# Kernel tuning notes

Hardware: AMD Instinct MI355X
Metric: run time of the kernel (lower is better)

Reference implementation:

```python
import jax, jax.numpy as jnp
import numpy as np

B, Q, N, C = 2, 1024, 4096, 768
H, D, REL = 12, 64, 32
SCALE = 1.0 / np.sqrt(D)


def _lin_coords(n_out, n_in):
    # align_corners=True mapping: x_in = x_out * (n_in-1)/(n_out-1)
    pos = jnp.arange(n_out, dtype=jnp.float32) * ((n_in - 1) / (n_out - 1))
    lo = jnp.clip(jnp.floor(pos).astype(jnp.int32), 0, n_in - 1)
    hi = jnp.clip(lo + 1, 0, n_in - 1)
    w = pos - lo.astype(jnp.float32)
    return lo, hi, w


def _interp_bias(bias, q_len, n_len):
    # bias: [H, 32, 32] -> [H, q_len, n_len] bilinear, align_corners=True
    lq, hq, wq = _lin_coords(q_len, REL)
    ln, hn, wn = _lin_coords(n_len, REL)
    b1 = bias[:, lq, :] * (1.0 - wq)[None, :, None] + bias[:, hq, :] * wq[None, :, None]  # [H,q,32]
    b2 = b1[:, :, ln] * (1.0 - wn)[None, None, :] + b1[:, :, hn] * wn[None, None, :]      # [H,q,n]
    return b2


def setup_inputs() -> dict:
    key = jax.random.key(0)
    ks = jax.random.split(key, 11)
    s = 1.0 / np.sqrt(C)
    return {
        "query": jax.random.normal(ks[0], (B, Q, C), jnp.float32),
        "key_value": jax.random.normal(ks[1], (B, N, C), jnp.float32),
        "Wq": jax.random.normal(ks[2], (C, C), jnp.float32) * s,
        "bq": jax.random.normal(ks[3], (C,), jnp.float32) * 0.01,
        "Wk": jax.random.normal(ks[4], (C, C), jnp.float32) * s,
        "bk": jax.random.normal(ks[5], (C,), jnp.float32) * 0.01,
        "Wv": jax.random.normal(ks[6], (C, C), jnp.float32) * s,
        "bv": jax.random.normal(ks[7], (C,), jnp.float32) * 0.01,
        "Wo": jax.random.normal(ks[8], (C, C), jnp.float32) * s,
        "bo": jax.random.normal(ks[9], (C,), jnp.float32) * 0.01,
        "rel_pos_bias": jax.random.normal(ks[10], (H, REL, REL), jnp.float32) * 0.02,
    }


def reference(query, key_value, Wq, bq, Wk, bk, Wv, bv, Wo, bo, rel_pos_bias):
    b, n, c = key_value.shape
    q_len = query.shape[1]
    # projections (dropout in eval mode -> identity)
    q = (query @ Wq + bq).reshape(b, q_len, H, D).transpose(0, 2, 1, 3)      # [B,H,Q,D]
    k = (key_value @ Wk + bk).reshape(b, n, H, D).transpose(0, 2, 1, 3)      # [B,H,N,D]
    v = (key_value @ Wv + bv).reshape(b, n, H, D).transpose(0, 2, 1, 3)      # [B,H,N,D]
    attn = jnp.einsum('bhqd,bhnd->bhqn', q, k) * SCALE
    attn = attn + _interp_bias(rel_pos_bias, q_len, n)[None]                 # [B,H,Q,N]
    p = jax.nn.softmax(attn, axis=-1)
    out = jnp.einsum('bhqn,bhnd->bhqd', p, v)
    out = out.transpose(0, 2, 1, 3).reshape(b, q_len, c)
    return out @ Wo + bo
```

## Files before the change

kernel.cpp:

```cpp
#include <hip/hip_runtime.h>
#include <stdint.h>

typedef unsigned short ushort_t;
typedef __bf16 bf16x8 __attribute__((ext_vector_type(8)));
typedef float f32x4 __attribute__((ext_vector_type(4)));
typedef unsigned short us4 __attribute__((ext_vector_type(4)));

#define LOG2E 1.4426950408889634f
#define NEG8L (-11.541560327111707f)
#define QSCALE 0.18033688011110974f

__device__ __forceinline__ ushort_t f2b(float f) {
    unsigned u = __float_as_uint(f);
    unsigned r = (u + 0x7fffu + ((u >> 16) & 1u)) >> 16;
    return (ushort_t)r;
}
__device__ __forceinline__ void gld16(const void* g, void* l) {
    __builtin_amdgcn_global_load_lds(
        (__attribute__((address_space(1))) void*)g,
        (__attribute__((address_space(3))) void*)l,
        16, 0, 0);
}

__global__ __launch_bounds__(256) void prep(
        const float* __restrict__ query, const float* __restrict__ keyv,
        const float* __restrict__ Wq, const float* __restrict__ Wk,
        const float* __restrict__ Wv, const float* __restrict__ Wo,
        const float* __restrict__ rel,
        ushort_t* __restrict__ qc, ushort_t* __restrict__ kvc,
        ushort_t* __restrict__ wtq, ushort_t* __restrict__ wtk,
        ushort_t* __restrict__ wtv, ushort_t* __restrict__ wto,
        ushort_t* __restrict__ b1b, ushort_t* __restrict__ wtab) {
    __shared__ ushort_t tsh[32][33];
    const int bid = blockIdx.x, tid = threadIdx.x;
    if (bid < 7680) {
        const float* src = (bid < 1536) ? query : keyv;
        ushort_t* dst = (bid < 1536) ? qc : kvc;
        int i = ((bid < 1536) ? bid : bid - 1536) * 256 + tid;
        float4 x = ((const float4*)src)[i];
        us4 v; v.x = f2b(x.x); v.y = f2b(x.y); v.z = f2b(x.z); v.w = f2b(x.w);
        ((us4*)dst)[i] = v;
    } else if (bid < 9984) {
        int t = bid - 7680, w = t / 576, tt = t - w * 576;
        const float* in = (w == 0) ? Wq : (w == 1) ? Wk : (w == 2) ? Wv : Wo;
        ushort_t* out = (w == 0) ? wtq : (w == 1) ? wtk : (w == 2) ? wtv : wto;
        int x = tid & 31, y = tid >> 5;
        int bx = (tt % 24) * 32, by = (tt / 24) * 32;
#pragma unroll
        for (int j = 0; j < 32; j += 8)
            tsh[y + j][x] = f2b(in[(size_t)(by + y + j) * 768 + bx + x]);
        __syncthreads();
#pragma unroll
        for (int j = 0; j < 32; j += 8)
            out[(size_t)(bx + y + j) * 768 + by + x] = tsh[x][y + j];
    } else if (bid < 11520) {
        int idx = (bid - 9984) * 256 + tid;
        int j = idx & 31, q = (idx >> 5) & 1023, h = idx >> 15;
        float pos = q * (31.0f / 1023.0f);
        float fl = floorf(pos);
        int lo = (int)fl; if (lo > 31) lo = 31;
        float w = pos - fl;
        int hi = lo + 1; if (hi > 31) hi = 31;
        float vlo = rel[(h * 32 + lo) * 32 + j];
        float vhi = rel[(h * 32 + hi) * 32 + j];
        b1b[idx] = f2b((vlo + (vhi - vlo) * w) * LOG2E);
    } else {
        int n = (bid - 11520) * 256 + tid;
        float pos = n * (31.0f / 4095.0f);
        float fl = floorf(pos);
        int ln = (int)fl; if (ln > 31) ln = 31;
        float wn = pos - fl;
        int hn = ln + 1; if (hn > 31) hn = 31;
        float vals[32];
#pragma unroll
        for (int j = 0; j < 32; ++j) vals[j] = 0.f;
        vals[ln] += 1.0f - wn;
        vals[hn] += wn;
#pragma unroll
        for (int j = 0; j < 32; ++j) wtab[n * 32 + j] = f2b(vals[j]);
    }
}

__device__ __forceinline__ void gemm_store(float bvf, f32x4 a, void* out,
                                           int mode, int lsh, float scale,
                                           int mbase, int n) {
    if (mode == 0) {
#pragma unroll
        for (int r = 0; r < 4; ++r)
            ((float*)out)[(size_t)(mbase + r) * 768 + n] = (a[r] + bvf) * scale;
    } else if (mode == 1) {
        int h = n >> 6, d = n & 63;
#pragma unroll
        for (int r = 0; r < 4; ++r) {
            int m = mbase + r;
            int b = m >> lsh, l = m & ((1 << lsh) - 1);
            ((ushort_t*)out)[((size_t)(((b * 12 + h) << lsh) + l) << 6) + d] = f2b((a[r] + bvf) * scale);
        }
    } else {
        int h = n >> 6, d = n & 63;
        int b = mbase >> lsh, l = mbase & ((1 << lsh) - 1);
        us4 v;
        v.x = f2b((a[0] + bvf) * scale);
        v.y = f2b((a[1] + bvf) * scale);
        v.z = f2b((a[2] + bvf) * scale);
        v.w = f2b((a[3] + bvf) * scale);
        *(us4*)((ushort_t*)out + ((size_t)((b * 12 + h) * 64 + d) << lsh) + l) = v;
    }
}

__device__ __forceinline__ void gemm_body128(const ushort_t* __restrict__ A,
                                             const ushort_t* __restrict__ Bt,
                                             const float* __restrict__ bias,
                                             void* __restrict__ out,
                                             int mode, int lsh, float scale,
                                             int m0, int n0,
                                             ushort_t* As, ushort_t* Bs, int tid) {
    const int wave = tid >> 6, lane = tid & 63;
    const int quad = lane >> 4, l15 = lane & 15;
    const int wm = wave >> 1, wn = wave & 1;
    const f32x4 z4 = {0.f, 0.f, 0.f, 0.f};
    f32x4 acc[4][4];
#pragma unroll
    for (int i = 0; i < 4; ++i)
#pragma unroll
        for (int j = 0; j < 4; ++j) acc[i][j] = z4;

    const int arow = lane >> 3;
    const int ablk = lane & 7;
    const int kswz = (ablk ^ arow) * 8;

    for (int kk = 0; kk < 768; kk += 64) {
        __syncthreads();
#pragma unroll
        for (int i = 0; i < 4; ++i) {
            int c = wave * 4 + i;
            gld16(A + (size_t)(m0 + c * 8 + arow) * 768 + kk + kswz, (void*)(As + c * 512));
            gld16(Bt + (size_t)(n0 + c * 8 + arow) * 768 + kk + kswz, (void*)(Bs + c * 512));
        }
        __syncthreads();
#pragma unroll
        for (int ks = 0; ks < 2; ++ks) {
            bf16x8 af[4], bf[4];
#pragma unroll
            for (int mb = 0; mb < 4; ++mb) {
                int r = wm * 64 + mb * 16 + l15;
                af[mb] = *(const bf16x8*)(As + r * 64 + (((ks * 4 + quad) ^ (r & 7)) * 8));
            }
#pragma unroll
            for (int nb = 0; nb < 4; ++nb) {
                int r = wn * 64 + nb * 16 + l15;
                bf[nb] = *(const bf16x8*)(Bs + r * 64 + (((ks * 4 + quad) ^ (r & 7)) * 8));
            }
#pragma unroll
            for (int mb = 0; mb < 4; ++mb)
#pragma unroll
                for (int nb = 0; nb < 4; ++nb)
                    acc[mb][nb] = __builtin_amdgcn_mfma_f32_16x16x32_bf16(af[mb], bf[nb], acc[mb][nb], 0, 0, 0);
        }
    }

#pragma unroll
    for (int mb = 0; mb < 4; ++mb) {
        int mbase = m0 + wm * 64 + mb * 16 + quad * 4;
#pragma unroll
        for (int nb = 0; nb < 4; ++nb) {
            int n = n0 + wn * 64 + nb * 16 + l15;
            gemm_store(bias[n], acc[mb][nb], out, mode, lsh, scale, mbase, n);
        }
    }
}

__device__ __forceinline__ void gemm_body64(const ushort_t* __restrict__ A,
                                            const ushort_t* __restrict__ Bt,
                                            const float* __restrict__ bias,
                                            void* __restrict__ out,
                                            int mode, int lsh, float scale,
                                            int m0, int n0,
                                            ushort_t* As, ushort_t* Bs, int tid) {
    const int wave = tid >> 6, lane = tid & 63;
    const int quad = lane >> 4, l15 = lane & 15;
    const f32x4 z4 = {0.f, 0.f, 0.f, 0.f};
    f32x4 acc[4];
#pragma unroll
    for (int j = 0; j < 4; ++j) acc[j] = z4;

    const int arow = lane >> 3;
    const int ablk = lane & 7;
    const int kswz = (ablk ^ arow) * 8;

    for (int kk = 0; kk < 768; kk += 64) {
        __syncthreads();
#pragma unroll
        for (int i = 0; i < 2; ++i) {
            int c = wave * 2 + i;
            gld16(A + (size_t)(m0 + c * 8 + arow) * 768 + kk + kswz, (void*)(As + c * 512));
            gld16(Bt + (size_t)(n0 + c * 8 + arow) * 768 + kk + kswz, (void*)(Bs + c * 512));
        }
        __syncthreads();
#pragma unroll
        for (int ks = 0; ks < 2; ++ks) {
            bf16x8 af, bf[4];
            {
                int r = wave * 16 + l15;
                af = *(const bf16x8*)(As + r * 64 + (((ks * 4 + quad) ^ (r & 7)) * 8));
            }
#pragma unroll
            for (int nb = 0; nb < 4; ++nb) {
                int r = nb * 16 + l15;
                bf[nb] = *(const bf16x8*)(Bs + r * 64 + (((ks * 4 + quad) ^ (r & 7)) * 8));
            }
#pragma unroll
            for (int nb = 0; nb < 4; ++nb)
                acc[nb] = __builtin_amdgcn_mfma_f32_16x16x32_bf16(af, bf[nb], acc[nb], 0, 0, 0);
        }
    }

    int mbase = m0 + wave * 16 + quad * 4;
#pragma unroll
    for (int nb = 0; nb < 4; ++nb) {
        int n = n0 + nb * 16 + l15;
        gemm_store(bias[n], acc[nb], out, mode, lsh, scale, mbase, n);
    }
}

__global__ __launch_bounds__(256) void proj3(const ushort_t* __restrict__ qc,
                                             const ushort_t* __restrict__ kvc,
                                             const ushort_t* __restrict__ wtq,
                                             const ushort_t* __restrict__ wtk,
                                             const ushort_t* __restrict__ wtv,
                                             const float* __restrict__ bq,
                                             const float* __restrict__ bk,
                                             const float* __restrict__ bv,
                                             ushort_t* __restrict__ qp,
                                             ushort_t* __restrict__ kp,
                                             ushort_t* __restrict__ vtp) {
    __shared__ __align__(16) ushort_t As[128 * 64];
    __shared__ __align__(16) ushort_t Bs[128 * 64];
    const int bid = blockIdx.x, tid = threadIdx.x;
    if (bid < 96) {
        int mt = bid & 15, nt = bid >> 4;
        gemm_body128(qc, wtq, bq, qp, 1, 10, QSCALE, mt * 128, nt * 128, As, Bs, tid);
    } else if (bid < 480) {
        int t = bid - 96, mt = t & 63, nt = t >> 6;
        gemm_body128(kvc, wtk, bk, kp, 1, 12, 1.0f, mt * 128, nt * 128, As, Bs, tid);
    } else {
        int t = bid - 480, mt = t & 63, nt = t >> 6;
        gemm_body128(kvc, wtv, bv, vtp, 2, 12, 1.0f, mt * 128, nt * 128, As, Bs, tid);
    }
}

__global__ __launch_bounds__(256) void gemm_out(const ushort_t* __restrict__ ab,
                                                const ushort_t* __restrict__ wto,
                                                const float* __restrict__ bo,
                                                float* __restrict__ out) {
    __shared__ __align__(16) ushort_t As[64 * 64];
    __shared__ __align__(16) ushort_t Bs[64 * 64];
    const int bid = blockIdx.x, tid = threadIdx.x;
    int mt = bid & 31, nt = bid >> 5;
    gemm_body64(ab, wto, bo, out, 0, 0, 1.0f, mt * 64, nt * 64, As, Bs, tid);
}

__global__ __launch_bounds__(256) void attn64s(const ushort_t* __restrict__ qp,
                                               const ushort_t* __restrict__ kp,
                                               const ushort_t* __restrict__ vt,
                                               const ushort_t* __restrict__ b1b,
                                               const ushort_t* __restrict__ wtab,
                                               float* __restrict__ po,
                                               float* __restrict__ pl) {
    __shared__ __align__(16) ushort_t k_s[64 * 64];
    __shared__ __align__(16) ushort_t v_s[64 * 64];
    __shared__ __align__(16) float pf[4][576];

    const int tid = threadIdx.x;
    const int wave = tid >> 6, lane = tid & 63;
    const int quad = lane >> 4, l15 = lane & 15;
    const int bid = blockIdx.x;
    const int xcd = bid & 7;
    const int slot = bid >> 3;
    const int g = xcd + 8 * (slot >> 6);
    const int member = slot & 63;
    const int b = g / 12, h = g - b * 12;
    const int qt = member & 15, sp = member >> 4;
    const int q0 = qt * 64;
    const int bh = g;

    const ushort_t* qg = qp + ((size_t)bh * 1024 + q0) * 64;
    const ushort_t* kg = kp + (size_t)bh * 4096 * 64;
    const ushort_t* vg = vt + (size_t)bh * 64 * 4096;

    const int rowq = wave * 16 + l15;
    bf16x8 aq[2];
#pragma unroll
    for (int ks = 0; ks < 2; ++ks)
        aq[ks] = *(const bf16x8*)(qg + (size_t)rowq * 64 + (ks * 4 + quad) * 8);
    bf16x8 ab1 = *(const bf16x8*)(b1b + ((size_t)(h * 1024 + q0 + rowq)) * 32 + quad * 8);

    const f32x4 mC = {NEG8L, NEG8L, NEG8L, NEG8L};
    const f32x4 z4 = {0.f, 0.f, 0.f, 0.f};
    f32x4 o[4];
    float lsum[4];
#pragma unroll
    for (int d = 0; d < 4; ++d) o[d] = z4;
#pragma unroll
    for (int r = 0; r < 4; ++r) lsum[r] = 0.f;

    const int arow = lane >> 3;
    const int ablk = lane & 7;

    for (int nt = 0; nt < 16; ++nt) {
        const int n0 = sp * 1024 + nt * 64;
        __syncthreads();
#pragma unroll
        for (int i = 0; i < 2; ++i) {
            int c = wave * 2 + i;
            int row = c * 8 + arow;
            int k16 = ablk ^ (row & 7);
            gld16(kg + (size_t)(n0 + row) * 64 + k16 * 8, (void*)(k_s + c * 512));
            gld16(vg + (size_t)row * 4096 + n0 + k16 * 8, (void*)(v_s + c * 512));
        }
        __syncthreads();

        bf16x8 wf[4];
#pragma unroll
        for (int nb = 0; nb < 4; ++nb)
            wf[nb] = *(const bf16x8*)(wtab + (size_t)(n0 + nb * 16 + l15) * 32 + quad * 8);

        f32x4 s[4];
#pragma unroll
        for (int nb = 0; nb < 4; ++nb) {
            s[nb] = __builtin_amdgcn_mfma_f32_16x16x32_bf16(ab1, wf[nb], mC, 0, 0, 0);
#pragma unroll
            for (int ks = 0; ks < 2; ++ks) {
                int rn = nb * 16 + l15;
                bf16x8 bk = *(const bf16x8*)(k_s + rn * 64 + (((ks * 4 + quad) ^ (rn & 7)) * 8));
                s[nb] = __builtin_amdgcn_mfma_f32_16x16x32_bf16(aq[ks], bk, s[nb], 0, 0, 0);
            }
        }
#pragma unroll
        for (int nb = 0; nb < 4; ++nb)
#pragma unroll
            for (int r = 0; r < 4; ++r) {
                float p = exp2f(s[nb][r]);
                s[nb][r] = p;
                lsum[r] += p;
            }
#pragma unroll
        for (int p = 0; p < 2; ++p) {
#pragma unroll
            for (int i = 0; i < 2; ++i) {
                int nb = 2 * p + i;
                float* dst = &pf[wave][(i * 16 + l15) * 18 + quad * 4];
                *(float2*)dst = make_float2(s[nb][0], s[nb][1]);
                *(float2*)(dst + 2) = make_float2(s[nb][2], s[nb][3]);
            }
            bf16x8 ap;
#pragma unroll
            for (int j = 0; j < 8; ++j)
                ap[j] = (__bf16)pf[wave][(quad * 8 + j) * 18 + l15];
#pragma unroll
            for (int d = 0; d < 4; ++d) {
                int rd = d * 16 + l15;
                bf16x8 bv = *(const bf16x8*)(v_s + rd * 64 + (((p * 4 + quad) ^ (rd & 7)) * 8));
                o[d] = __builtin_amdgcn_mfma_f32_16x16x32_bf16(ap, bv, o[d], 0, 0, 0);
            }
        }
    }

#pragma unroll
    for (int r = 0; r < 4; ++r)
#pragma unroll
        for (int off = 1; off < 16; off <<= 1)
            lsum[r] += __shfl_xor(lsum[r], off, 64);

    const size_t pbase = ((size_t)(sp * 24 + bh)) * 1024;
#pragma unroll
    for (int r = 0; r < 4; ++r) {
        int qrow = q0 + wave * 16 + quad * 4 + r;
        if (l15 == 0) pl[pbase + qrow] = lsum[r];
#pragma unroll
        for (int d = 0; d < 4; ++d)
            po[(pbase + qrow) * 64 + d * 16 + l15] = o[d][r];
    }
}

__global__ __launch_bounds__(256) void combine(const float* __restrict__ po,
                                               const float* __restrict__ pl,
                                               ushort_t* __restrict__ ab) {
    int idx = blockIdx.x * 256 + threadIdx.x;
    int e = idx * 4;
    int b = e / 786432;
    int rem = e - b * 786432;
    int q = rem / 768;
    int col = rem - q * 768;
    int h = col >> 6, d = col & 63;
    int bh = b * 12 + h;
    float4 acc = {0.f, 0.f, 0.f, 0.f};
    float l = 0.f;
#pragma unroll
    for (int s = 0; s < 4; ++s) {
        size_t base = ((size_t)(s * 24 + bh)) * 1024 + q;
        float4 v = *(const float4*)(po + base * 64 + d);
        acc.x += v.x; acc.y += v.y; acc.z += v.z; acc.w += v.w;
        l += pl[base];
    }
    float inv = 1.0f / l;
    us4 v;
    v.x = f2b(acc.x * inv); v.y = f2b(acc.y * inv);
    v.z = f2b(acc.z * inv); v.w = f2b(acc.w * inv);
    *(us4*)(ab + (size_t)(b * 1024 + q) * 768 + col) = v;
}

extern "C" void kernel_launch(void* const* d_in, const int* in_sizes, int n_in,
                              void* d_out, int out_size, void* d_ws, size_t ws_size,
                              hipStream_t stream) {
    const float* query = (const float*)d_in[0];
    const float* keyv  = (const float*)d_in[1];
    const float* Wq = (const float*)d_in[2];
    const float* bq = (const float*)d_in[3];
    const float* Wk = (const float*)d_in[4];
    const float* bk = (const float*)d_in[5];
    const float* Wv = (const float*)d_in[6];
    const float* bv = (const float*)d_in[7];
    const float* Wo = (const float*)d_in[8];
    const float* bo = (const float*)d_in[9];
    const float* rel = (const float*)d_in[10];

    char* ws = (char*)d_ws;
    ushort_t* qc   = (ushort_t*)(ws + 0);
    ushort_t* kvc  = (ushort_t*)(ws + 3145728);
    ushort_t* wtq  = (ushort_t*)(ws + 15728640);
    ushort_t* wtk  = (ushort_t*)(ws + 16908288);
    ushort_t* wtv  = (ushort_t*)(ws + 18087936);
    ushort_t* wto  = (ushort_t*)(ws + 19267584);
    ushort_t* qp   = (ushort_t*)(ws + 20447232);
    ushort_t* kp   = (ushort_t*)(ws + 23592960);
    ushort_t* vtp  = (ushort_t*)(ws + 36175872);
    ushort_t* b1b  = (ushort_t*)(ws + 48758784);
    ushort_t* wtab = (ushort_t*)(ws + 49545216);
    ushort_t* ab   = (ushort_t*)(ws + 49807360);
    float*    po   = (float*)(ws + 52953088);
    float*    pl   = (float*)(ws + 78118912);

    prep<<<11536, 256, 0, stream>>>(query, keyv, Wq, Wk, Wv, Wo, rel,
                                    qc, kvc, wtq, wtk, wtv, wto, b1b, wtab);
    proj3<<<864, 256, 0, stream>>>(qc, kvc, wtq, wtk, wtv, bq, bk, bv, qp, kp, vtp);
    attn64s<<<1536, 256, 0, stream>>>(qp, kp, vtp, b1b, wtab, po, pl);
    combine<<<1536, 256, 0, stream>>>(po, pl, ab);
    gemm_out<<<384, 256, 0, stream>>>(ab, wto, bo, (float*)d_out);
}
```

Before: 215.7 us.

## Swap GEMM operands for vectorized transposed stores, remap tiles, split attention launch

The Q/K projections and the output GEMM now compute the transposed product by swapping the A and B operands. Each lane then writes four contiguous outputs as one packed 8-byte bf16 or 16-byte float4 store, replacing scattered scalar stores. Tile indexing is remapped so that neighbouring blocks, which land on different XCDs, share operand tiles. The attention kernel is split into two launches that each cover half of the KV splits. The bias is now read per row at four addresses, and the split launch adds launch overhead and a serialization point between the halves.

After: 225.1 us. +4.4%, slower.

```diff
diff --git a/kernel.cpp b/kernel.cpp
--- a/kernel.cpp
+++ b/kernel.cpp
@@ -81,30 +81,36 @@
     }
 }
 
-__device__ __forceinline__ void gemm_store(float bvf, f32x4 a, void* out,
+__device__ __forceinline__ void gemm_store(const float* __restrict__ bias,
+                                           f32x4 a, void* out,
                                            int mode, int lsh, float scale,
                                            int mbase, int n) {
-    if (mode == 0) {
-#pragma unroll
-        for (int r = 0; r < 4; ++r)
-            ((float*)out)[(size_t)(mbase + r) * 768 + n] = (a[r] + bvf) * scale;
-    } else if (mode == 1) {
-        int h = n >> 6, d = n & 63;
-#pragma unroll
-        for (int r = 0; r < 4; ++r) {
-            int m = mbase + r;
-            int b = m >> lsh, l = m & ((1 << lsh) - 1);
-            ((ushort_t*)out)[((size_t)(((b * 12 + h) << lsh) + l) << 6) + d] = f2b((a[r] + bvf) * scale);
-        }
-    } else {
+    if (mode == 2) {
         int h = n >> 6, d = n & 63;
         int b = mbase >> lsh, l = mbase & ((1 << lsh) - 1);
+        float bvf = bias[n];
         us4 v;
         v.x = f2b((a[0] + bvf) * scale);
         v.y = f2b((a[1] + bvf) * scale);
         v.z = f2b((a[2] + bvf) * scale);
         v.w = f2b((a[3] + bvf) * scale);
         *(us4*)((ushort_t*)out + ((size_t)((b * 12 + h) * 64 + d) << lsh) + l) = v;
+    } else if (mode == 3) {
+        int h = mbase >> 6, dbase = mbase & 63;
+        int b = n >> lsh, l = n & ((1 << lsh) - 1);
+        us4 v;
+        v.x = f2b((a[0] + bias[mbase + 0]) * scale);
+        v.y = f2b((a[1] + bias[mbase + 1]) * scale);
+        v.z = f2b((a[2] + bias[mbase + 2]) * scale);
+        v.w = f2b((a[3] + bias[mbase + 3]) * scale);
+        *(us4*)((ushort_t*)out + ((((size_t)(b * 12 + h) << lsh) + l) << 6) + dbase) = v;
+    } else {
+        float4 v;
+        v.x = (a[0] + bias[mbase + 0]) * scale;
+        v.y = (a[1] + bias[mbase + 1]) * scale;
+        v.z = (a[2] + bias[mbase + 2]) * scale;
+        v.w = (a[3] + bias[mbase + 3]) * scale;
+        *(float4*)((float*)out + (size_t)n * 768 + mbase) = v;
     }
 }
 
@@ -165,7 +171,7 @@
 #pragma unroll
         for (int nb = 0; nb < 4; ++nb) {
             int n = n0 + wn * 64 + nb * 16 + l15;
-            gemm_store(bias[n], acc[mb][nb], out, mode, lsh, scale, mbase, n);
+            gemm_store(bias, acc[mb][nb], out, mode, lsh, scale, mbase, n);
         }
     }
 }
@@ -219,7 +225,7 @@
 #pragma unroll
     for (int nb = 0; nb < 4; ++nb) {
         int n = n0 + nb * 16 + l15;
-        gemm_store(bias[n], acc[nb], out, mode, lsh, scale, mbase, n);
+        gemm_store(bias, acc[nb], out, mode, lsh, scale, mbase, n);
     }
 }
 
@@ -238,11 +244,13 @@
     __shared__ __align__(16) ushort_t Bs[128 * 64];
     const int bid = blockIdx.x, tid = threadIdx.x;
     if (bid < 96) {
-        int mt = bid & 15, nt = bid >> 4;
-        gemm_body128(qc, wtq, bq, qp, 1, 10, QSCALE, mt * 128, nt * 128, As, Bs, tid);
+        int t = bid;
+        int nt = (t & 7) + 8 * ((t >> 3) & 1), mt = t >> 4;
+        gemm_body128(wtq, qc, bq, qp, 3, 10, QSCALE, mt * 128, nt * 128, As, Bs, tid);
     } else if (bid < 480) {
-        int t = bid - 96, mt = t & 63, nt = t >> 6;
-        gemm_body128(kvc, wtk, bk, kp, 1, 12, 1.0f, mt * 128, nt * 128, As, Bs, tid);
+        int t = bid - 96;
+        int nt = (t & 7) + 8 * ((t >> 3) & 7), mt = t >> 6;
+        gemm_body128(wtk, kvc, bk, kp, 3, 12, 1.0f, mt * 128, nt * 128, As, Bs, tid);
     } else {
         int t = bid - 480, mt = t & 63, nt = t >> 6;
         gemm_body128(kvc, wtv, bv, vtp, 2, 12, 1.0f, mt * 128, nt * 128, As, Bs, tid);
@@ -256,8 +264,9 @@
     __shared__ __align__(16) ushort_t As[64 * 64];
     __shared__ __align__(16) ushort_t Bs[64 * 64];
     const int bid = blockIdx.x, tid = threadIdx.x;
-    int mt = bid & 31, nt = bid >> 5;
-    gemm_body64(ab, wto, bo, out, 0, 0, 1.0f, mt * 64, nt * 64, As, Bs, tid);
+    int j = bid >> 3;
+    int nt = (bid & 7) + 8 * (j & 3), mt = j >> 2;
+    gemm_body64(wto, ab, bo, out, 4, 0, 1.0f, mt * 64, nt * 64, As, Bs, tid);
 }
 
 __global__ __launch_bounds__(256) void attn64s(const ushort_t* __restrict__ qp,
@@ -266,7 +275,8 @@
                                                const ushort_t* __restrict__ b1b,
                                                const ushort_t* __restrict__ wtab,
                                                float* __restrict__ po,
-                                               float* __restrict__ pl) {
+                                               float* __restrict__ pl,
+                                               int sp_base) {
     __shared__ __align__(16) ushort_t k_s[64 * 64];
     __shared__ __align__(16) ushort_t v_s[64 * 64];
     __shared__ __align__(16) float pf[4][576];
@@ -277,10 +287,10 @@
     const int bid = blockIdx.x;
     const int xcd = bid & 7;
     const int slot = bid >> 3;
-    const int g = xcd + 8 * (slot >> 6);
-    const int member = slot & 63;
+    const int g = xcd + 8 * (slot >> 5);
+    const int member = slot & 31;
     const int b = g / 12, h = g - b * 12;
-    const int qt = member & 15, sp = member >> 4;
+    const int qt = member & 15, sp = sp_base + (member >> 4);
     const int q0 = qt * 64;
     const int bh = g;
 
@@ -444,7 +454,8 @@
     prep<<<11536, 256, 0, stream>>>(query, keyv, Wq, Wk, Wv, Wo, rel,
                                     qc, kvc, wtq, wtk, wtv, wto, b1b, wtab);
     proj3<<<864, 256, 0, stream>>>(qc, kvc, wtq, wtk, wtv, bq, bk, bv, qp, kp, vtp);
-    attn64s<<<1536, 256, 0, stream>>>(qp, kp, vtp, b1b, wtab, po, pl);
+    attn64s<<<768, 256, 0, stream>>>(qp, kp, vtp, b1b, wtab, po, pl, 0);
+    attn64s<<<768, 256, 0, stream>>>(qp, kp, vtp, b1b, wtab, po, pl, 2);
     combine<<<1536, 256, 0, stream>>>(po, pl, ab);
     gemm_out<<<384, 256, 0, stream>>>(ab, wto, bo, (float*)d_out);
 }
```
